# Kernel tuning notes

Measured on AMD Instinct MI355X. Metric: run time of the kernel, lower is better.

The kernel has to match this reference:

```python
import jax, jax.numpy as jnp
import numpy as np

N_CELLS = 1024
HID = 256
IN_DIM = 256
OUT_DIM = 256
NOISE_DIM = 32
N_LOOP = 32  # min(32, n_cells)


def _lin(x, W, b):
    # torch nn.Linear: y = x @ W.T + b, W shape [out, in]
    return x @ W.T + b


def faction_sync_debate(h, step, n_factions=8, sync=0.15, debate=0.15):
    n, d = h.shape
    n_f = min(n_factions, n // 2)
    if n_f < 2:
        return h
    fs = n // n_f  # assumes n_f * fs == n (true for 1024/8)
    blk = h.reshape(n_f, fs, d)
    # per-faction mean pull (disjoint slices -> order independent)
    blk = (1.0 - sync) * blk + sync * blk.mean(axis=1, keepdims=True)
    if step > 5:  # step is a Python int -> static branch
        global_opinion = blk.mean(axis=1).mean(axis=0)  # [d]
        dc = max(1, fs // 4)
        blk = blk.at[:, :dc, :].set((1.0 - debate) * blk[:, :dc, :] + debate * global_opinion)
    return blk.reshape(n, d)


def setup_inputs() -> dict:
    key = jax.random.key(0)
    ks = iter(jax.random.split(key, 32))

    def rn(shape, scale=0.02):
        return (jax.random.normal(next(ks), shape, dtype=jnp.float32) * scale)

    flat = N_CELLS * HID  # 262144
    inp = {
        "x": rn((1, IN_DIM), 1.0),
        "noise": rn((1, NOISE_DIM), 1.0),
        "cell_hiddens": rn((N_CELLS, HID), 0.1),
        # generator: Linear(in+32,256) -> ReLU -> Linear(256,512) -> ReLU -> Linear(512, flat)
        "gen_W1": rn((256, IN_DIM + NOISE_DIM)), "gen_b1": rn((256,)),
        "gen_W2": rn((512, 256)), "gen_b2": rn((512,)),
        "gen_W3": rn((flat, 512)), "gen_b3": rn((flat,)),
        # discriminator: Linear(flat,512) -> LReLU(0.2) -> Linear(512,256) -> LReLU -> Linear(256,1) -> Sigmoid
        "disc_W1": rn((512, flat)), "disc_b1": rn((512,)),
        "disc_W2": rn((256, 512)), "disc_b2": rn((256,)),
        "disc_W3": rn((1, 256)), "disc_b3": rn((1,)),
        # mind engines: Linear(in+hid,128) -> ReLU -> Linear(128,out)
        "ea_W1": rn((128, IN_DIM + HID)), "ea_b1": rn((128,)),
        "ea_W2": rn((OUT_DIM, 128)), "ea_b2": rn((OUT_DIM,)),
        "eg_W1": rn((128, IN_DIM + HID)), "eg_b1": rn((128,)),
        "eg_W2": rn((OUT_DIM, 128)), "eg_b2": rn((OUT_DIM,)),
        # GRUCell(out+1, hid): gate order r, z, n
        "gru_Wih": rn((3 * HID, OUT_DIM + 1)), "gru_bih": rn((3 * HID,)),
        "gru_Whh": rn((3 * HID, HID)), "gru_bhh": rn((3 * HID,)),
        "step": 10,
    }
    return inp


def reference(x, noise, cell_hiddens,
              gen_W1, gen_b1, gen_W2, gen_b2, gen_W3, gen_b3,
              disc_W1, disc_b1, disc_W2, disc_b2, disc_W3, disc_b3,
              ea_W1, ea_b1, ea_W2, ea_b2, eg_W1, eg_b1, eg_W2, eg_b2,
              gru_Wih, gru_bih, gru_Whh, gru_bhh, step):
    sg = jax.lax.stop_gradient
    # --- generate_states ---
    gi = jnp.concatenate([x, noise], axis=-1)           # [1, in+32]
    h1 = jax.nn.relu(_lin(gi, gen_W1, gen_b1))
    h2 = jax.nn.relu(_lin(h1, gen_W2, gen_b2))
    gen_states = _lin(h2, gen_W3, gen_b3).reshape(N_CELLS, HID)
    # torch: gen_states.detach() then faction sync+debate
    synced = faction_sync_debate(sg(gen_states), step)
    # --- batched BenchMind over first 32 cells (replaces Python loop) ---
    H = synced[:N_LOOP]                                  # [32, HID]
    X = jnp.broadcast_to(x, (N_LOOP, x.shape[-1]))       # [32, IN]
    comb = jnp.concatenate([X, H], axis=-1)              # [32, IN+HID]
    a = _lin(jax.nn.relu(_lin(comb, ea_W1, ea_b1)), ea_W2, ea_b2)
    g = _lin(jax.nn.relu(_lin(comb, eg_W1, eg_b1)), eg_W2, eg_b2)
    outputs = a - g                                      # [32, OUT]
    tensions = (outputs ** 2).mean(axis=-1)              # [32]
    # GRUCell update (mem inputs detached as in torch)
    mem_in = jnp.concatenate([sg(outputs), sg(tensions)[:, None]], axis=-1)  # [32, OUT+1]
    gih = _lin(mem_in, gru_Wih, gru_bih)
    ghh = _lin(H, gru_Whh, gru_bhh)
    ir, iz, i_n = jnp.split(gih, 3, axis=-1)
    hr, hz, h_n = jnp.split(ghh, 3, axis=-1)
    r = jax.nn.sigmoid(ir + hr)
    z = jax.nn.sigmoid(iz + hz)
    n_cand = jnp.tanh(i_n + r * h_n)
    new_hiddens = (1.0 - z) * n_cand + z * H             # [32, HID]
    # --- buffer update (no_grad) + discriminate ---
    new_cell_hiddens = sg(0.7 * synced + 0.3 * cell_hiddens)

    def disc(s):
        f = s.reshape(1, -1)
        d1 = jax.nn.leaky_relu(_lin(f, disc_W1, disc_b1), 0.2)
        d2 = jax.nn.leaky_relu(_lin(d1, disc_W2, disc_b2), 0.2)
        return jax.nn.sigmoid(_lin(d2, disc_W3, disc_b3))

    d_real = disc(new_cell_hiddens)
    d_fake = disc(gen_states)
    # tensions were .item()'d in torch -> constants
    mean_tension = sg(tensions).mean()
    w = jax.nn.softmax(sg(tensions))                     # [32]
    combined = (w[:, None] * outputs).sum(axis=0, keepdims=True)  # [1, OUT]
    return combined, mean_tension, d_real, d_fake, new_hiddens
```

## Files before the change

kernel.cpp:

```cpp
#include <hip/hip_runtime.h>
#include <math.h>

#define N_CELLS 1024
#define HID     256
#define IN_DIM  256
#define NOISE_DIM 32
#define OUT_DIM 256
#define N_LOOP  32
#define FLAT    (N_CELLS*HID)

typedef float f4 __attribute__((ext_vector_type(4)));

__device__ __forceinline__ float wave_reduce64(float v) {
    #pragma unroll
    for (int m = 32; m; m >>= 1) v += __shfl_xor(v, m);
    return v;
}
__device__ __forceinline__ float dot4(float4 a, float4 b) {
    return a.x*b.x + a.y*b.y + a.z*b.z + a.w*b.w;
}
__device__ __forceinline__ float dot4v(f4 a, float4 b) {
    return a.x*b.x + a.y*b.y + a.z*b.z + a.w*b.w;
}
__device__ __forceinline__ float dot4vv(f4 a, f4 b) {
    return a.x*b.x + a.y*b.y + a.z*b.z + a.w*b.w;
}

__global__ void k_gen_h1(const float* __restrict__ x, const float* __restrict__ noise,
                         const float* __restrict__ W1, const float* __restrict__ b1,
                         float* __restrict__ h1) {
    __shared__ __align__(16) float gi[288];
    int t = threadIdx.x, l = t & 63, w = t >> 6;
    gi[t] = x[t];
    if (t < 32) gi[256 + t] = noise[t];
    __syncthreads();
    int j = blockIdx.x * 4 + w;
    const float4* wr = (const float4*)(W1 + j * 288);
    const float4* g4 = (const float4*)gi;
    float4 a = wr[l], v = g4[l];
    float acc = dot4(a, v);
    if (l < 8) {
        float4 a2 = wr[64 + l], v2 = g4[64 + l];
        acc += dot4(a2, v2);
    }
    acc = wave_reduce64(acc);
    if (l == 0) h1[j] = fmaxf(acc + b1[j], 0.f);
}

__global__ void k_gen_h2(const float* __restrict__ h1, const float* __restrict__ W2,
                         const float* __restrict__ b2, float* __restrict__ h2) {
    int t = threadIdx.x, l = t & 63, w = t >> 6;
    int j = blockIdx.x * 4 + w;
    float4 a = ((const float4*)(W2 + j * 256))[l];
    float4 v = ((const float4*)h1)[l];
    float acc = dot4(a, v);
    acc = wave_reduce64(acc);
    if (l == 0) h2[j] = fmaxf(acc + b2[j], 0.f);
}

__global__ void k_gen_big(const float* __restrict__ W3, const float* __restrict__ b3,
                          const float* __restrict__ h2, float* __restrict__ gs) {
    int t = threadIdx.x, l = t & 63, w = t >> 6;
    int r0 = blockIdx.x * 16 + w * 4;
    const float4* h24 = (const float4*)h2;
    float4 ha = h24[l], hb = h24[64 + l];
    const f4* w0 = (const f4*)(W3 + (size_t)(r0 + 0) * 512);
    const f4* w1 = (const f4*)(W3 + (size_t)(r0 + 1) * 512);
    const f4* w2 = (const f4*)(W3 + (size_t)(r0 + 2) * 512);
    const f4* w3 = (const f4*)(W3 + (size_t)(r0 + 3) * 512);
    f4 A0 = __builtin_nontemporal_load(w0 + l);
    f4 B0 = __builtin_nontemporal_load(w0 + 64 + l);
    f4 A1 = __builtin_nontemporal_load(w1 + l);
    f4 B1 = __builtin_nontemporal_load(w1 + 64 + l);
    f4 A2 = __builtin_nontemporal_load(w2 + l);
    f4 B2 = __builtin_nontemporal_load(w2 + 64 + l);
    f4 A3 = __builtin_nontemporal_load(w3 + l);
    f4 B3 = __builtin_nontemporal_load(w3 + 64 + l);
    float s0 = dot4v(A0, ha) + dot4v(B0, hb);
    float s1 = dot4v(A1, ha) + dot4v(B1, hb);
    float s2 = dot4v(A2, ha) + dot4v(B2, hb);
    float s3 = dot4v(A3, ha) + dot4v(B3, hb);
    s0 = wave_reduce64(s0);
    s1 = wave_reduce64(s1);
    s2 = wave_reduce64(s2);
    s3 = wave_reduce64(s3);
    if (l == 0) {
        float4 bv = *(const float4*)(b3 + r0);
        float4 o; o.x = s0 + bv.x; o.y = s1 + bv.y; o.z = s2 + bv.z; o.w = s3 + bv.w;
        *(float4*)(gs + r0) = o;
    }
}

__global__ void k_fmean(const float* __restrict__ gs, float* __restrict__ fmean) {
    __shared__ float part[4][64];
    int b = blockIdx.x, t = threadIdx.x;
    int f = b >> 2, q = b & 3;
    int c = q * 64 + (t & 63), rg = t >> 6;
    const float* base = gs + (size_t)(f * 128 + rg * 32) * 256 + c;
    float s0 = 0.f, s1 = 0.f, s2 = 0.f, s3 = 0.f;
    for (int i = 0; i < 32; i += 4) {
        s0 += base[(size_t)(i + 0) * 256];
        s1 += base[(size_t)(i + 1) * 256];
        s2 += base[(size_t)(i + 2) * 256];
        s3 += base[(size_t)(i + 3) * 256];
    }
    part[rg][t & 63] = (s0 + s1) + (s2 + s3);
    __syncthreads();
    if (t < 64) {
        float v = part[0][t] + part[1][t] + part[2][t] + part[3][t];
        fmean[f * 256 + q * 64 + t] = v * (1.f / 128.f);
    }
}

__global__ void k_mega(const float* __restrict__ dW1, const float* __restrict__ db1,
                       const float* __restrict__ gs, const float* __restrict__ ch,
                       const float* __restrict__ fmean, const int* __restrict__ step,
                       const float* __restrict__ x,
                       const float* __restrict__ eaW1, const float* __restrict__ eab1,
                       const float* __restrict__ eaW2, const float* __restrict__ eab2,
                       const float* __restrict__ egW1, const float* __restrict__ egb1,
                       const float* __restrict__ egW2, const float* __restrict__ egb2,
                       const float* __restrict__ Wih, const float* __restrict__ bih,
                       const float* __restrict__ Whh, const float* __restrict__ bhh,
                       float* __restrict__ d1r, float* __restrict__ d1f,
                       float* __restrict__ outputs, float* __restrict__ tensions,
                       float* __restrict__ out) {
    __shared__ float sR[16];
    __shared__ float sF[16];
    __shared__ __align__(16) float fmL[2048];
    __shared__ __align__(16) float gmL[256];
    __shared__ __align__(16) float xh[512];
    __shared__ __align__(16) float hag[256];
    __shared__ __align__(16) float outs[256];
    __shared__ float red[256];
    __shared__ float rzA[512];
    __shared__ float inb[256];
    __shared__ float hnb[256];
    __shared__ float tsh;
    int b = blockIdx.x, t = threadIdx.x, l = t & 63, w = t >> 6;
    bool deb = (*step > 5);

    if (b >= 32) {
        for (int i = t; i < 2048; i += 1024) fmL[i] = fmean[i];
        __syncthreads();
        if (t < 256) {
            float g = 0.f;
            #pragma unroll
            for (int f = 0; f < 8; ++f) g += fmL[f * 256 + t];
            gmL[t] = g * 0.125f;
        }
        __syncthreads();
        int row = b - 32;
        const f4* w4 = (const f4*)(dW1 + (size_t)row * FLAT);
        const float4* g4 = (const float4*)gs;
        const float4* c4 = (const float4*)ch;
        float aR = 0.f, aF = 0.f;
        for (int i = t; i < FLAT / 4; i += 1024) {
            int c = i >> 6, d4 = i & 63;
            f4 ww = __builtin_nontemporal_load(w4 + i);
            float4 gv = g4[i], cv = c4[i];
            float4 fmv = *(const float4*)(fmL + ((c >> 7) << 8) + d4 * 4);
            float4 v;
            v.x = 0.85f * gv.x + 0.15f * fmv.x;
            v.y = 0.85f * gv.y + 0.15f * fmv.y;
            v.z = 0.85f * gv.z + 0.15f * fmv.z;
            v.w = 0.85f * gv.w + 0.15f * fmv.w;
            if (deb && ((c & 127) < 32)) {
                float4 gm = *(const float4*)(gmL + d4 * 4);
                v.x = 0.85f * v.x + 0.15f * gm.x;
                v.y = 0.85f * v.y + 0.15f * gm.y;
                v.z = 0.85f * v.z + 0.15f * gm.z;
                v.w = 0.85f * v.w + 0.15f * gm.w;
            }
            float4 nc;
            nc.x = 0.7f * v.x + 0.3f * cv.x;
            nc.y = 0.7f * v.y + 0.3f * cv.y;
            nc.z = 0.7f * v.z + 0.3f * cv.z;
            nc.w = 0.7f * v.w + 0.3f * cv.w;
            aR += dot4v(ww, nc);
            aF += dot4v(ww, gv);
        }
        aR = wave_reduce64(aR);
        aF = wave_reduce64(aF);
        if (l == 0) { sR[w] = aR; sF[w] = aF; }
        __syncthreads();
        if (t < 16) {
            float r = sR[t], f = sF[t];
            #pragma unroll
            for (int m = 8; m; m >>= 1) { r += __shfl_xor(r, m); f += __shfl_xor(f, m); }
            if (t == 0) { d1r[row] = r + db1[row]; d1f[row] = f + db1[row]; }
        }
        return;
    }

    int i = b;
    if (t < 256) {
        xh[t] = x[t];
        float g = gs[i * 256 + t];
        float gmv = 0.f;
        #pragma unroll
        for (int f = 0; f < 8; ++f) gmv += fmean[f * 256 + t];
        gmv *= 0.125f;
        float v = 0.85f * g + 0.15f * fmean[t];
        if (deb) v = 0.85f * v + 0.15f * gmv;
        xh[256 + t] = v;
    }
    __syncthreads();

    for (int k = 0; k < 16; ++k) {
        int j = w * 16 + k;
        const float* W = (j < 128) ? (eaW1 + (size_t)j * 512) : (egW1 + (size_t)(j - 128) * 512);
        const float4* w4 = (const float4*)W;
        const float4* v4 = (const float4*)xh;
        float acc = dot4(w4[l], v4[l]) + dot4(w4[64 + l], v4[64 + l]);
        acc = wave_reduce64(acc);
        if (l == 0) {
            float bias = (j < 128) ? eab1[j] : egb1[j - 128];
            hag[j] = fmaxf(acc + bias, 0.f);
        }
    }
    __syncthreads();

    for (int k = 0; k < 16; ++k) {
        int tr = w * 16 + k;
        int sl = l & 31;
        bool lo = (l < 32);
        const float4* wv4 = lo ? (const float4*)(eaW2 + (size_t)tr * 128)
                               : (const float4*)(egW2 + (size_t)tr * 128);
        const float4* h4 = (const float4*)(hag + (lo ? 0 : 128));
        float d_ = dot4(wv4[sl], h4[sl]);
        float acc = lo ? d_ : -d_;
        acc = wave_reduce64(acc);
        if (l == 0) {
            float o = acc + eab2[tr] - egb2[tr];
            outs[tr] = o;
            outputs[i * 256 + tr] = o;
        }
    }
    __syncthreads();

    if (t < 256) red[t] = outs[t] * outs[t];
    __syncthreads();
    for (int m = 128; m; m >>= 1) { if (t < m && t + m < 256) red[t] += red[t + m]; __syncthreads(); }
    if (t == 0) { float tn = red[0] * (1.f / 256.f); tensions[i] = tn; tsh = tn; }
    __syncthreads();
    float tn = tsh;

    {
        float4 ov = ((const float4*)outs)[l];
        float4 Hv = ((const float4*)(xh + 256))[l];
        for (int k = 0; k < 48; ++k) {
            int u = w * 48 + k;
            const float* wr = Wih + (size_t)u * 257;
            float g0 = wr[4*l]*ov.x + wr[4*l+1]*ov.y + wr[4*l+2]*ov.z + wr[4*l+3]*ov.w;
            if (l == 0) g0 += wr[256] * tn;
            float4 wh = ((const float4*)(Whh + (size_t)u * 256))[l];
            float h0 = dot4(wh, Hv);
            if (u < 512) {
                float s = wave_reduce64(g0 + h0);
                if (l == 0) rzA[u] = s + bih[u] + bhh[u];
            } else {
                float sg = wave_reduce64(g0);
                float sh = wave_reduce64(h0);
                if (l == 0) { inb[u - 512] = sg + bih[u]; hnb[u - 512] = sh + bhh[u]; }
            }
        }
    }
    __syncthreads();

    if (t < 256) {
        float r = 1.f / (1.f + expf(-rzA[t]));
        float z = 1.f / (1.f + expf(-rzA[256 + t]));
        float nc = tanhf(inb[t] + r * hnb[t]);
        float Hd = xh[256 + t];
        out[259 + i * 256 + t] = (1.f - z) * nc + z * Hd;
    }
}

__global__ void k_epi1(const float* __restrict__ W2, const float* __restrict__ b2,
                       const float* __restrict__ d1r, const float* __restrict__ d1f,
                       float* __restrict__ l2buf) {
    __shared__ __align__(16) float lv[512];
    int b = blockIdx.x, t = threadIdx.x, l = t & 63, w = t >> 6;
    int br = b >> 2, q = b & 3;
    const float* d1 = br ? d1f : d1r;
    for (int j = t; j < 512; j += 256) { float v = d1[j]; lv[j] = v > 0.f ? v : 0.2f * v; }
    __syncthreads();
    const float4* l4 = (const float4*)lv;
    float4 va = l4[l], vb = l4[64 + l];
    for (int k = 0; k < 16; ++k) {
        int tr = q * 64 + w * 16 + k;
        const float4* wr = (const float4*)(W2 + (size_t)tr * 512);
        float acc = dot4(wr[l], va) + dot4(wr[64 + l], vb);
        acc = wave_reduce64(acc);
        if (l == 0) {
            float z = acc + b2[tr];
            l2buf[br * 256 + tr] = z > 0.f ? z : 0.2f * z;
        }
    }
}

__global__ void k_epi2(const float* __restrict__ W3, const float* __restrict__ b3,
                       const float* __restrict__ l2buf,
                       const float* __restrict__ outputs, const float* __restrict__ tensions,
                       float* __restrict__ out) {
    __shared__ float red[256];
    __shared__ float w[32];
    __shared__ float ts[32];
    int t = threadIdx.x;
    for (int p = 0; p < 2; ++p) {
        red[t] = l2buf[p * 256 + t] * W3[t];
        __syncthreads();
        for (int m = 128; m; m >>= 1) { if (t < m) red[t] += red[t + m]; __syncthreads(); }
        if (t == 0) out[257 + p] = 1.f / (1.f + expf(-(red[0] + b3[0])));
        __syncthreads();
    }
    if (t < 32) ts[t] = tensions[t];
    __syncthreads();
    if (t == 0) {
        float mx = ts[0];
        for (int i = 1; i < 32; ++i) mx = fmaxf(mx, ts[i]);
        float s = 0.f, mean = 0.f;
        for (int i = 0; i < 32; ++i) { float e = expf(ts[i] - mx); w[i] = e; s += e; mean += ts[i]; }
        float inv = 1.f / s;
        for (int i = 0; i < 32; ++i) w[i] *= inv;
        out[256] = mean * (1.f / 32.f);
    }
    __syncthreads();
    float c = 0.f;
    for (int i = 0; i < 32; ++i) c += w[i] * outputs[i * 256 + t];
    out[t] = c;
}

extern "C" void kernel_launch(void* const* d_in, const int* in_sizes, int n_in,
                              void* d_out, int out_size, void* d_ws, size_t ws_size,
                              hipStream_t stream) {
    const float* x     = (const float*)d_in[0];
    const float* noise = (const float*)d_in[1];
    const float* ch    = (const float*)d_in[2];
    const float* gW1   = (const float*)d_in[3];
    const float* gb1   = (const float*)d_in[4];
    const float* gW2   = (const float*)d_in[5];
    const float* gb2   = (const float*)d_in[6];
    const float* gW3   = (const float*)d_in[7];
    const float* gb3   = (const float*)d_in[8];
    const float* dW1   = (const float*)d_in[9];
    const float* db1   = (const float*)d_in[10];
    const float* dW2   = (const float*)d_in[11];
    const float* db2   = (const float*)d_in[12];
    const float* dW3   = (const float*)d_in[13];
    const float* db3   = (const float*)d_in[14];
    const float* eaW1  = (const float*)d_in[15];
    const float* eab1  = (const float*)d_in[16];
    const float* eaW2  = (const float*)d_in[17];
    const float* eab2  = (const float*)d_in[18];
    const float* egW1  = (const float*)d_in[19];
    const float* egb1  = (const float*)d_in[20];
    const float* egW2  = (const float*)d_in[21];
    const float* egb2  = (const float*)d_in[22];
    const float* Wih   = (const float*)d_in[23];
    const float* bih   = (const float*)d_in[24];
    const float* Whh   = (const float*)d_in[25];
    const float* bhh   = (const float*)d_in[26];
    const int*   step  = (const int*)d_in[27];

    float* out = (float*)d_out;
    float* ws  = (float*)d_ws;
    float* h1buf    = ws;
    float* h2       = h1buf + 256;
    float* gs       = h2 + 512;
    float* fmean    = gs + 262144;
    float* outputs  = fmean + 2048;
    float* tensions = outputs + 8192;
    float* d1r      = tensions + 32;
    float* d1f      = d1r + 512;
    float* l2buf    = d1f + 512;

    k_gen_h1<<<64, 256, 0, stream>>>(x, noise, gW1, gb1, h1buf);
    k_gen_h2<<<128, 256, 0, stream>>>(h1buf, gW2, gb2, h2);
    k_gen_big<<<FLAT / 16, 256, 0, stream>>>(gW3, gb3, h2, gs);
    k_fmean<<<32, 256, 0, stream>>>(gs, fmean);
    k_mega<<<544, 1024, 0, stream>>>(dW1, db1, gs, ch, fmean, step, x,
                                     eaW1, eab1, eaW2, eab2,
                                     egW1, egb1, egW2, egb2,
                                     Wih, bih, Whh, bhh,
                                     d1r, d1f, outputs, tensions, out);
    k_epi1<<<8, 256, 0, stream>>>(dW2, db2, d1r, d1f, l2buf);
    k_epi2<<<1, 256, 0, stream>>>(dW3, db3, l2buf, outputs, tensions, out);
}
```

Baseline: 274.2 us.

## Fuse generator GEMV, faction means and discriminator into one flag-synchronized kernel

Merges the big generator GEMV, the per-faction mean and the discriminator/GRU work into one persistent-style launch. Interleaved consumer blocks wait on per-faction atomic flags, so streaming the 512MB discriminator weights overlaps with streaming the generator weights. Each discriminator block now handles two rows and shares the gs/ch loads between them. The synced state is folded algebraically into the dot-product coefficients, with a separate debate-sum correction. The cost is spin-wait dependencies on block scheduling order, which can deadlock or stall if consumer blocks occupy all slots before their producers run, plus relaxed atomic loads of gs.

```diff
diff --git a/kernel.cpp b/kernel.cpp
--- a/kernel.cpp
+++ b/kernel.cpp
@@ -3,11 +3,11 @@
 
 #define N_CELLS 1024
 #define HID     256
-#define IN_DIM  256
-#define NOISE_DIM 32
-#define OUT_DIM 256
 #define N_LOOP  32
 #define FLAT    (N_CELLS*HID)
+
+#define GRIDF   4384
+#define NSPEC   288
 
 typedef float f4 __attribute__((ext_vector_type(4)));
 
@@ -22,27 +22,24 @@
 __device__ __forceinline__ float dot4v(f4 a, float4 b) {
     return a.x*b.x + a.y*b.y + a.z*b.z + a.w*b.w;
 }
-__device__ __forceinline__ float dot4vv(f4 a, f4 b) {
-    return a.x*b.x + a.y*b.y + a.z*b.z + a.w*b.w;
-}
+
+#define ALD(p)   __hip_atomic_load((p), __ATOMIC_RELAXED, __HIP_MEMORY_SCOPE_AGENT)
+#define AST(p,v) __hip_atomic_store((p), (v), __ATOMIC_RELAXED, __HIP_MEMORY_SCOPE_AGENT)
 
 __global__ void k_gen_h1(const float* __restrict__ x, const float* __restrict__ noise,
                          const float* __restrict__ W1, const float* __restrict__ b1,
-                         float* __restrict__ h1) {
+                         float* __restrict__ h1, unsigned int* __restrict__ ctrl) {
     __shared__ __align__(16) float gi[288];
     int t = threadIdx.x, l = t & 63, w = t >> 6;
+    if (blockIdx.x == 0 && t < 64) ctrl[t] = 0u;
     gi[t] = x[t];
     if (t < 32) gi[256 + t] = noise[t];
     __syncthreads();
     int j = blockIdx.x * 4 + w;
     const float4* wr = (const float4*)(W1 + j * 288);
     const float4* g4 = (const float4*)gi;
-    float4 a = wr[l], v = g4[l];
-    float acc = dot4(a, v);
-    if (l < 8) {
-        float4 a2 = wr[64 + l], v2 = g4[64 + l];
-        acc += dot4(a2, v2);
-    }
+    float acc = dot4(wr[l], g4[l]);
+    if (l < 8) acc += dot4(wr[64 + l], g4[64 + l]);
     acc = wave_reduce64(acc);
     if (l == 0) h1[j] = fmaxf(acc + b1[j], 0.f);
 }
@@ -51,229 +48,296 @@
                          const float* __restrict__ b2, float* __restrict__ h2) {
     int t = threadIdx.x, l = t & 63, w = t >> 6;
     int j = blockIdx.x * 4 + w;
-    float4 a = ((const float4*)(W2 + j * 256))[l];
-    float4 v = ((const float4*)h1)[l];
-    float acc = dot4(a, v);
+    float acc = dot4(((const float4*)(W2 + j * 256))[l], ((const float4*)h1)[l]);
     acc = wave_reduce64(acc);
     if (l == 0) h2[j] = fmaxf(acc + b2[j], 0.f);
 }
 
-__global__ void k_gen_big(const float* __restrict__ W3, const float* __restrict__ b3,
-                          const float* __restrict__ h2, float* __restrict__ gs) {
-    int t = threadIdx.x, l = t & 63, w = t >> 6;
-    int r0 = blockIdx.x * 16 + w * 4;
-    const float4* h24 = (const float4*)h2;
-    float4 ha = h24[l], hb = h24[64 + l];
-    const f4* w0 = (const f4*)(W3 + (size_t)(r0 + 0) * 512);
-    const f4* w1 = (const f4*)(W3 + (size_t)(r0 + 1) * 512);
-    const f4* w2 = (const f4*)(W3 + (size_t)(r0 + 2) * 512);
-    const f4* w3 = (const f4*)(W3 + (size_t)(r0 + 3) * 512);
-    f4 A0 = __builtin_nontemporal_load(w0 + l);
-    f4 B0 = __builtin_nontemporal_load(w0 + 64 + l);
-    f4 A1 = __builtin_nontemporal_load(w1 + l);
-    f4 B1 = __builtin_nontemporal_load(w1 + 64 + l);
-    f4 A2 = __builtin_nontemporal_load(w2 + l);
-    f4 B2 = __builtin_nontemporal_load(w2 + 64 + l);
-    f4 A3 = __builtin_nontemporal_load(w3 + l);
-    f4 B3 = __builtin_nontemporal_load(w3 + 64 + l);
-    float s0 = dot4v(A0, ha) + dot4v(B0, hb);
-    float s1 = dot4v(A1, ha) + dot4v(B1, hb);
-    float s2 = dot4v(A2, ha) + dot4v(B2, hb);
-    float s3 = dot4v(A3, ha) + dot4v(B3, hb);
-    s0 = wave_reduce64(s0);
-    s1 = wave_reduce64(s1);
-    s2 = wave_reduce64(s2);
-    s3 = wave_reduce64(s3);
-    if (l == 0) {
-        float4 bv = *(const float4*)(b3 + r0);
-        float4 o; o.x = s0 + bv.x; o.y = s1 + bv.y; o.z = s2 + bv.z; o.w = s3 + bv.w;
-        *(float4*)(gs + r0) = o;
-    }
-}
-
-__global__ void k_fmean(const float* __restrict__ gs, float* __restrict__ fmean) {
-    __shared__ float part[4][64];
-    int b = blockIdx.x, t = threadIdx.x;
-    int f = b >> 2, q = b & 3;
-    int c = q * 64 + (t & 63), rg = t >> 6;
-    const float* base = gs + (size_t)(f * 128 + rg * 32) * 256 + c;
-    float s0 = 0.f, s1 = 0.f, s2 = 0.f, s3 = 0.f;
-    for (int i = 0; i < 32; i += 4) {
-        s0 += base[(size_t)(i + 0) * 256];
-        s1 += base[(size_t)(i + 1) * 256];
-        s2 += base[(size_t)(i + 2) * 256];
-        s3 += base[(size_t)(i + 3) * 256];
-    }
-    part[rg][t & 63] = (s0 + s1) + (s2 + s3);
-    __syncthreads();
-    if (t < 64) {
-        float v = part[0][t] + part[1][t] + part[2][t] + part[3][t];
-        fmean[f * 256 + q * 64 + t] = v * (1.f / 128.f);
-    }
-}
-
-__global__ void k_mega(const float* __restrict__ dW1, const float* __restrict__ db1,
-                       const float* __restrict__ gs, const float* __restrict__ ch,
-                       const float* __restrict__ fmean, const int* __restrict__ step,
-                       const float* __restrict__ x,
-                       const float* __restrict__ eaW1, const float* __restrict__ eab1,
-                       const float* __restrict__ eaW2, const float* __restrict__ eab2,
-                       const float* __restrict__ egW1, const float* __restrict__ egb1,
-                       const float* __restrict__ egW2, const float* __restrict__ egb2,
-                       const float* __restrict__ Wih, const float* __restrict__ bih,
-                       const float* __restrict__ Whh, const float* __restrict__ bhh,
-                       float* __restrict__ d1r, float* __restrict__ d1f,
-                       float* __restrict__ outputs, float* __restrict__ tensions,
-                       float* __restrict__ out) {
-    __shared__ float sR[16];
-    __shared__ float sF[16];
+__global__ void __launch_bounds__(1024, 8)
+k_fused(const float* __restrict__ W3, const float* __restrict__ b3,
+        const float* __restrict__ h2,
+        const float* __restrict__ dW1, const float* __restrict__ db1,
+        const float* __restrict__ ch, const int* __restrict__ step,
+        const float* __restrict__ x,
+        const float* __restrict__ eaW1, const float* __restrict__ eab1,
+        const float* __restrict__ eaW2, const float* __restrict__ eab2,
+        const float* __restrict__ egW1, const float* __restrict__ egb1,
+        const float* __restrict__ egW2, const float* __restrict__ egb2,
+        const float* __restrict__ Wih, const float* __restrict__ bih,
+        const float* __restrict__ Whh, const float* __restrict__ bhh,
+        float* __restrict__ gs, float* __restrict__ fmean,
+        unsigned int* __restrict__ ctrl,
+        float* __restrict__ d1r, float* __restrict__ d1f,
+        float* __restrict__ outputs, float* __restrict__ tensions,
+        float* __restrict__ out) {
     __shared__ __align__(16) float fmL[2048];
     __shared__ __align__(16) float gmL[256];
-    __shared__ __align__(16) float xh[512];
+    __shared__ __align__(16) float swl[4096];
+    __shared__ float swS[256];
+    __shared__ float sA[16], sB[16], sC[16], sD[16];
+    __shared__ float sS[2];
+    __shared__ __align__(16) float fm_part[1024];
+    __shared__ int lastS;
+    __shared__ __align__(16) float xL[256];
+    __shared__ __align__(16) float vf[256];
+    __shared__ float Hacc[256];
+    __shared__ float E[256];
+    __shared__ float Ghh[768];
     __shared__ __align__(16) float hag[256];
     __shared__ __align__(16) float outs[256];
     __shared__ float red[256];
-    __shared__ float rzA[512];
-    __shared__ float inb[256];
-    __shared__ float hnb[256];
+    __shared__ float gihL[768];
     __shared__ float tsh;
+
+    unsigned int* fcnt  = ctrl;
+    unsigned int* fflag = ctrl + 32;
     int b = blockIdx.x, t = threadIdx.x, l = t & 63, w = t >> 6;
     bool deb = (*step > 5);
 
-    if (b >= 32) {
-        for (int i = t; i < 2048; i += 1024) fmL[i] = fmean[i];
+    int s = -1;
+    if ((b % 15) == 0 && (b / 15) < NSPEC) s = b / 15;
+
+    if (s < 0) {
+        int nb = (b == 0) ? 0 : ((b - 1) / 15 + 1);
+        if (nb > NSPEC) nb = NSPEC;
+        int g = b - nb;
+        int fct = g >> 9;
+        int r0 = g * 64 + w * 4;
+        const float4* h24 = (const float4*)h2;
+        float4 ha = h24[l], hb = h24[64 + l];
+        const f4* w0p = (const f4*)(W3 + (size_t)(r0 + 0) * 512);
+        const f4* w1p = (const f4*)(W3 + (size_t)(r0 + 1) * 512);
+        const f4* w2p = (const f4*)(W3 + (size_t)(r0 + 2) * 512);
+        const f4* w3p = (const f4*)(W3 + (size_t)(r0 + 3) * 512);
+        f4 A0 = __builtin_nontemporal_load(w0p + l), B0 = __builtin_nontemporal_load(w0p + 64 + l);
+        f4 A1 = __builtin_nontemporal_load(w1p + l), B1 = __builtin_nontemporal_load(w1p + 64 + l);
+        f4 A2 = __builtin_nontemporal_load(w2p + l), B2 = __builtin_nontemporal_load(w2p + 64 + l);
+        f4 A3 = __builtin_nontemporal_load(w3p + l), B3 = __builtin_nontemporal_load(w3p + 64 + l);
+        float s0 = dot4v(A0, ha) + dot4v(B0, hb);
+        float s1 = dot4v(A1, ha) + dot4v(B1, hb);
+        float s2 = dot4v(A2, ha) + dot4v(B2, hb);
+        float s3 = dot4v(A3, ha) + dot4v(B3, hb);
+        s0 = wave_reduce64(s0); s1 = wave_reduce64(s1);
+        s2 = wave_reduce64(s2); s3 = wave_reduce64(s3);
+        if (l < 4) {
+            float sv = (l == 0) ? s0 : (l == 1) ? s1 : (l == 2) ? s2 : s3;
+            AST(gs + r0 + l, sv + b3[r0 + l]);
+        }
+        __syncthreads();
+        if (t == 0)
+            lastS = (__hip_atomic_fetch_add(&fcnt[fct], 1u, __ATOMIC_ACQ_REL,
+                                            __HIP_MEMORY_SCOPE_AGENT) == 511u);
+        __syncthreads();
+        if (lastS) {
+            int d = t & 255, q = t >> 8;
+            const float* basep = gs + fct * 32768 + q * 8192 + d;
+            float sum = 0.f;
+            for (int r = 0; r < 32; ++r) sum += ALD(basep + r * 256);
+            fm_part[t] = sum;
+            __syncthreads();
+            if (t < 256) {
+                float v = (fm_part[t] + fm_part[256 + t] + fm_part[512 + t] + fm_part[768 + t])
+                          * (1.f / 128.f);
+                AST(fmean + fct * 256 + t, v);
+            }
+            __syncthreads();
+            if (t == 0)
+                __hip_atomic_store(&fflag[fct], 1u, __ATOMIC_RELEASE, __HIP_MEMORY_SCOPE_AGENT);
+        }
+        return;
+    }
+
+    if (s < 256) {
+        int row0 = 2 * s, row1 = 2 * s + 1;
+        const f4* wr0 = (const f4*)dW1 + (size_t)row0 * 65536;
+        const f4* wr1 = (const f4*)dW1 + (size_t)row1 * 65536;
+        const float4* c4 = (const float4*)ch;
+        float aR0 = 0.f, aF0 = 0.f, aR1 = 0.f, aF1 = 0.f;
+        f4 SW0 = {0.f, 0.f, 0.f, 0.f}, SW1 = {0.f, 0.f, 0.f, 0.f};
+        for (int f = 0; f < 8; ++f) {
+            if (t == 0) {
+                while (__hip_atomic_load(&fflag[f], __ATOMIC_ACQUIRE,
+                                         __HIP_MEMORY_SCOPE_AGENT) == 0u)
+                    __builtin_amdgcn_s_sleep(16);
+            }
+            __syncthreads();
+            if (t < 256) fmL[f * 256 + t] = ALD(fmean + f * 256 + t);
+            __syncthreads();
+            int base = f * 8192;
+            #pragma unroll 2
+            for (int k2 = 0; k2 < 8; ++k2) {
+                int i = base + k2 * 1024 + t;
+                f4 ww0 = __builtin_nontemporal_load(wr0 + i);
+                f4 ww1 = __builtin_nontemporal_load(wr1 + i);
+                const float* gp = gs + 4 * (size_t)i;
+                float g0 = ALD(gp + 0), g1 = ALD(gp + 1), g2 = ALD(gp + 2), g3 = ALD(gp + 3);
+                float4 cv = c4[i];
+                f4 fmv = ((const f4*)fmL)[(f << 6) + (i & 63)];
+                bool debate = deb && (((i >> 6) & 127) < 32);
+                float cg = debate ? 0.50575f : 0.595f;
+                float cf = debate ? 0.08925f : 0.105f;
+                float dg0 = ww0.x*g0 + ww0.y*g1 + ww0.z*g2 + ww0.w*g3;
+                float df0 = ww0.x*fmv.x + ww0.y*fmv.y + ww0.z*fmv.z + ww0.w*fmv.w;
+                float dc0 = ww0.x*cv.x + ww0.y*cv.y + ww0.z*cv.z + ww0.w*cv.w;
+                aR0 += cg*dg0 + cf*df0 + 0.3f*dc0;  aF0 += dg0;
+                float dg1 = ww1.x*g0 + ww1.y*g1 + ww1.z*g2 + ww1.w*g3;
+                float df1 = ww1.x*fmv.x + ww1.y*fmv.y + ww1.z*fmv.z + ww1.w*fmv.w;
+                float dc1 = ww1.x*cv.x + ww1.y*cv.y + ww1.z*cv.z + ww1.w*cv.w;
+                aR1 += cg*dg1 + cf*df1 + 0.3f*dc1;  aF1 += dg1;
+                if (debate) { SW0 += ww0; SW1 += ww1; }
+            }
+        }
         __syncthreads();
         if (t < 256) {
-            float g = 0.f;
+            float gsum = 0.f;
             #pragma unroll
-            for (int f = 0; f < 8; ++f) g += fmL[f * 256 + t];
-            gmL[t] = g * 0.125f;
-        }
-        __syncthreads();
-        int row = b - 32;
-        const f4* w4 = (const f4*)(dW1 + (size_t)row * FLAT);
-        const float4* g4 = (const float4*)gs;
-        const float4* c4 = (const float4*)ch;
-        float aR = 0.f, aF = 0.f;
-        for (int i = t; i < FLAT / 4; i += 1024) {
-            int c = i >> 6, d4 = i & 63;
-            f4 ww = __builtin_nontemporal_load(w4 + i);
-            float4 gv = g4[i], cv = c4[i];
-            float4 fmv = *(const float4*)(fmL + ((c >> 7) << 8) + d4 * 4);
-            float4 v;
-            v.x = 0.85f * gv.x + 0.15f * fmv.x;
-            v.y = 0.85f * gv.y + 0.15f * fmv.y;
-            v.z = 0.85f * gv.z + 0.15f * fmv.z;
-            v.w = 0.85f * gv.w + 0.15f * fmv.w;
-            if (deb && ((c & 127) < 32)) {
-                float4 gm = *(const float4*)(gmL + d4 * 4);
-                v.x = 0.85f * v.x + 0.15f * gm.x;
-                v.y = 0.85f * v.y + 0.15f * gm.y;
-                v.z = 0.85f * v.z + 0.15f * gm.z;
-                v.w = 0.85f * v.w + 0.15f * gm.w;
-            }
-            float4 nc;
-            nc.x = 0.7f * v.x + 0.3f * cv.x;
-            nc.y = 0.7f * v.y + 0.3f * cv.y;
-            nc.z = 0.7f * v.z + 0.3f * cv.z;
-            nc.w = 0.7f * v.w + 0.3f * cv.w;
-            aR += dot4v(ww, nc);
-            aF += dot4v(ww, gv);
-        }
-        aR = wave_reduce64(aR);
-        aF = wave_reduce64(aF);
-        if (l == 0) { sR[w] = aR; sF[w] = aF; }
+            for (int f = 0; f < 8; ++f) gsum += fmL[f * 256 + t];
+            gmL[t] = gsum * 0.125f;
+        }
+        __syncthreads();
+        ((f4*)swl)[w * 64 + l] = SW0;
+        __syncthreads();
+        if (t < 256) {
+            float sv = 0.f;
+            #pragma unroll
+            for (int q = 0; q < 16; ++q) sv += swl[q * 256 + t];
+            swS[t] = sv * gmL[t];
+        }
+        __syncthreads();
+        for (int m = 128; m; m >>= 1) { if (t < m) swS[t] += swS[t + m]; __syncthreads(); }
+        if (t == 0) sS[0] = swS[0];
+        __syncthreads();
+        ((f4*)swl)[w * 64 + l] = SW1;
+        __syncthreads();
+        if (t < 256) {
+            float sv = 0.f;
+            #pragma unroll
+            for (int q = 0; q < 16; ++q) sv += swl[q * 256 + t];
+            swS[t] = sv * gmL[t];
+        }
+        __syncthreads();
+        for (int m = 128; m; m >>= 1) { if (t < m) swS[t] += swS[t + m]; __syncthreads(); }
+        if (t == 0) sS[1] = swS[0];
+        __syncthreads();
+        aR0 = wave_reduce64(aR0); aF0 = wave_reduce64(aF0);
+        aR1 = wave_reduce64(aR1); aF1 = wave_reduce64(aF1);
+        if (l == 0) { sA[w] = aR0; sB[w] = aF0; sC[w] = aR1; sD[w] = aF1; }
         __syncthreads();
         if (t < 16) {
-            float r = sR[t], f = sF[t];
+            float a = sA[t], bb = sB[t], c = sC[t], dd = sD[t];
             #pragma unroll
-            for (int m = 8; m; m >>= 1) { r += __shfl_xor(r, m); f += __shfl_xor(f, m); }
-            if (t == 0) { d1r[row] = r + db1[row]; d1f[row] = f + db1[row]; }
+            for (int m = 8; m; m >>= 1) {
+                a += __shfl_xor(a, m); bb += __shfl_xor(bb, m);
+                c += __shfl_xor(c, m); dd += __shfl_xor(dd, m);
+            }
+            if (t == 0) {
+                d1r[row0] = a + 0.105f * sS[0] + db1[row0];
+                d1f[row0] = bb + db1[row0];
+                d1r[row1] = c + 0.105f * sS[1] + db1[row1];
+                d1f[row1] = dd + db1[row1];
+            }
         }
         return;
     }
 
-    int i = b;
-    if (t < 256) {
-        xh[t] = x[t];
-        float g = gs[i * 256 + t];
-        float gmv = 0.f;
-        #pragma unroll
-        for (int f = 0; f < 8; ++f) gmv += fmean[f * 256 + t];
-        gmv *= 0.125f;
-        float v = 0.85f * g + 0.15f * fmean[t];
-        if (deb) v = 0.85f * v + 0.15f * gmv;
-        xh[256 + t] = v;
-    }
-    __syncthreads();
-
-    for (int k = 0; k < 16; ++k) {
-        int j = w * 16 + k;
-        const float* W = (j < 128) ? (eaW1 + (size_t)j * 512) : (egW1 + (size_t)(j - 128) * 512);
-        const float4* w4 = (const float4*)W;
-        const float4* v4 = (const float4*)xh;
-        float acc = dot4(w4[l], v4[l]) + dot4(w4[64 + l], v4[64 + l]);
-        acc = wave_reduce64(acc);
-        if (l == 0) {
-            float bias = (j < 128) ? eab1[j] : egb1[j - 128];
-            hag[j] = fmaxf(acc + bias, 0.f);
-        }
-    }
-    __syncthreads();
-
-    for (int k = 0; k < 16; ++k) {
-        int tr = w * 16 + k;
-        int sl = l & 31;
-        bool lo = (l < 32);
-        const float4* wv4 = lo ? (const float4*)(eaW2 + (size_t)tr * 128)
-                               : (const float4*)(egW2 + (size_t)tr * 128);
-        const float4* h4 = (const float4*)(hag + (lo ? 0 : 128));
-        float d_ = dot4(wv4[sl], h4[sl]);
-        float acc = lo ? d_ : -d_;
-        acc = wave_reduce64(acc);
-        if (l == 0) {
-            float o = acc + eab2[tr] - egb2[tr];
-            outs[tr] = o;
-            outputs[i * 256 + tr] = o;
-        }
-    }
-    __syncthreads();
-
-    if (t < 256) red[t] = outs[t] * outs[t];
-    __syncthreads();
-    for (int m = 128; m; m >>= 1) { if (t < m && t + m < 256) red[t] += red[t + m]; __syncthreads(); }
-    if (t == 0) { float tn = red[0] * (1.f / 256.f); tensions[i] = tn; tsh = tn; }
-    __syncthreads();
-    float tn = tsh;
-
     {
-        float4 ov = ((const float4*)outs)[l];
-        float4 Hv = ((const float4*)(xh + 256))[l];
-        for (int k = 0; k < 48; ++k) {
-            int u = w * 48 + k;
-            const float* wr = Wih + (size_t)u * 257;
-            float g0 = wr[4*l]*ov.x + wr[4*l+1]*ov.y + wr[4*l+2]*ov.z + wr[4*l+3]*ov.w;
-            if (l == 0) g0 += wr[256] * tn;
-            float4 wh = ((const float4*)(Whh + (size_t)u * 256))[l];
-            float h0 = dot4(wh, Hv);
-            if (u < 512) {
-                float s = wave_reduce64(g0 + h0);
-                if (l == 0) rzA[u] = s + bih[u] + bhh[u];
-            } else {
-                float sg = wave_reduce64(g0);
-                float sh = wave_reduce64(h0);
-                if (l == 0) { inb[u - 512] = sg + bih[u]; hnb[u - 512] = sh + bhh[u]; }
-            }
-        }
-    }
-    __syncthreads();
-
-    if (t < 256) {
-        float r = 1.f / (1.f + expf(-rzA[t]));
-        float z = 1.f / (1.f + expf(-rzA[256 + t]));
-        float nc = tanhf(inb[t] + r * hnb[t]);
-        float Hd = xh[256 + t];
-        out[259 + i * 256 + t] = (1.f - z) * nc + z * Hd;
+        int i = s - 256;
+        if (t < 256) { xL[t] = x[t]; Hacc[t] = 0.f; }
+        for (int j2 = t; j2 < 768; j2 += 1024) Ghh[j2] = 0.f;
+        __syncthreads();
+        for (int k = 0; k < 16; ++k) {
+            int j = w * 16 + k;
+            const float* Wp = (j < 128) ? (eaW1 + (size_t)j * 512)
+                                        : (egW1 + (size_t)(j - 128) * 512);
+            float acc = dot4(((const float4*)Wp)[l], ((const float4*)xL)[l]);
+            acc = wave_reduce64(acc);
+            if (l == 0) E[j] = acc;
+        }
+        int nf = deb ? 8 : 1;
+        for (int f = 0; f < nf; ++f) {
+            if (t == 0) {
+                while (__hip_atomic_load(&fflag[f], __ATOMIC_ACQUIRE,
+                                         __HIP_MEMORY_SCOPE_AGENT) == 0u)
+                    __builtin_amdgcn_s_sleep(16);
+            }
+            __syncthreads();
+            if (t < 256) {
+                float fmv = ALD(fmean + f * 256 + t);
+                float v;
+                if (f == 0) {
+                    float gsv = ALD(gs + i * 256 + t);
+                    v = deb ? (0.7225f * gsv + 0.14625f * fmv)
+                            : (0.85f * gsv + 0.15f * fmv);
+                } else {
+                    v = 0.01875f * fmv;
+                }
+                vf[t] = v;
+                Hacc[t] += v;
+            }
+            __syncthreads();
+            for (int k = 0; k < 16; ++k) {
+                int j = w * 16 + k;
+                const float* Wp = (j < 128) ? (eaW1 + (size_t)j * 512 + 256)
+                                            : (egW1 + (size_t)(j - 128) * 512 + 256);
+                float acc = dot4(((const float4*)Wp)[l], ((const float4*)vf)[l]);
+                acc = wave_reduce64(acc);
+                if (l == 0) E[j] += acc;
+            }
+            for (int k = 0; k < 48; ++k) {
+                int u = w * 48 + k;
+                float acc = dot4(((const float4*)(Whh + (size_t)u * 256))[l],
+                                 ((const float4*)vf)[l]);
+                acc = wave_reduce64(acc);
+                if (l == 0) Ghh[u] += acc;
+            }
+            __syncthreads();
+        }
+        if (t < 256) {
+            float e = E[t] + ((t < 128) ? eab1[t] : egb1[t - 128]);
+            hag[t] = fmaxf(e, 0.f);
+        }
+        __syncthreads();
+        for (int k = 0; k < 16; ++k) {
+            int tr = w * 16 + k;
+            int sl = l & 31;
+            bool lo = (l < 32);
+            const float4* wv4 = lo ? (const float4*)(eaW2 + (size_t)tr * 128)
+                                   : (const float4*)(egW2 + (size_t)tr * 128);
+            const float4* h4 = (const float4*)(hag + (lo ? 0 : 128));
+            float d_ = dot4(wv4[sl], h4[sl]);
+            float acc = lo ? d_ : -d_;
+            acc = wave_reduce64(acc);
+            if (l == 0) {
+                float o = acc + eab2[tr] - egb2[tr];
+                outs[tr] = o;
+                outputs[i * 256 + tr] = o;
+            }
+        }
+        __syncthreads();
+        if (t < 256) red[t] = outs[t] * outs[t];
+        __syncthreads();
+        for (int m = 128; m; m >>= 1) { if (t < m) red[t] += red[t + m]; __syncthreads(); }
+        if (t == 0) { float tn = red[0] * (1.f / 256.f); tensions[i] = tn; tsh = tn; }
+        __syncthreads();
+        float tn = tsh;
+        {
+            float4 ov = ((const float4*)outs)[l];
+            for (int k = 0; k < 48; ++k) {
+                int u = w * 48 + k;
+                const float* wr = Wih + (size_t)u * 257;
+                float g0 = wr[4*l]*ov.x + wr[4*l+1]*ov.y + wr[4*l+2]*ov.z + wr[4*l+3]*ov.w;
+                if (l == 0) g0 += wr[256] * tn;
+                g0 = wave_reduce64(g0);
+                if (l == 0) gihL[u] = g0 + bih[u];
+            }
+        }
+        __syncthreads();
+        if (t < 256) {
+            float rr = 1.f / (1.f + expf(-(gihL[t] + Ghh[t] + bhh[t])));
+            float zz = 1.f / (1.f + expf(-(gihL[256 + t] + Ghh[256 + t] + bhh[256 + t])));
+            float ncand = tanhf(gihL[512 + t] + rr * (Ghh[512 + t] + bhh[512 + t]));
+            out[259 + i * 256 + t] = (1.f - zz) * ncand + zz * Hacc[t];
+        }
     }
 }
 
@@ -375,16 +439,17 @@
     float* d1r      = tensions + 32;
     float* d1f      = d1r + 512;
     float* l2buf    = d1f + 512;
-
-    k_gen_h1<<<64, 256, 0, stream>>>(x, noise, gW1, gb1, h1buf);
+    unsigned int* ctrl = (unsigned int*)(l2buf + 512);
+
+    k_gen_h1<<<64, 256, 0, stream>>>(x, noise, gW1, gb1, h1buf, ctrl);
     k_gen_h2<<<128, 256, 0, stream>>>(h1buf, gW2, gb2, h2);
-    k_gen_big<<<FLAT / 16, 256, 0, stream>>>(gW3, gb3, h2, gs);
-    k_fmean<<<32, 256, 0, stream>>>(gs, fmean);
-    k_mega<<<544, 1024, 0, stream>>>(dW1, db1, gs, ch, fmean, step, x,
-                                     eaW1, eab1, eaW2, eab2,
-                                     egW1, egb1, egW2, egb2,
-                                     Wih, bih, Whh, bhh,
-                                     d1r, d1f, outputs, tensions, out);
+    k_fused<<<GRIDF, 1024, 0, stream>>>(gW3, gb3, h2,
+                                        dW1, db1, ch, step, x,
+                                        eaW1, eab1, eaW2, eab2,
+                                        egW1, egb1, egW2, egb2,
+                                        Wih, bih, Whh, bhh,
+                                        gs, fmean, ctrl,
+                                        d1r, d1f, outputs, tensions, out);
     k_epi1<<<8, 256, 0, stream>>>(dW2, db2, d1r, d1f, l2buf);
     k_epi2<<<1, 256, 0, stream>>>(dW3, db3, l2buf, outputs, tensions, out);
 }
```

Measured after the change: 709.2 us. 2.59x slower.

## Process two discriminator rows per block over half the columns to reuse state loads

Applied to the files above, without the earlier changes.

Each discriminator block now handles two weight rows over half of the flattened input instead of one full row, so the recomputed synced/new-hidden values and gs/ch loads are shared across two rows. Partial sums for each half are written to scratch, and the bias add plus the combining of the halves move into k_epi1. k_fmean is also rewritten to use 8 blocks with float4 column reads. The intent is to cut redundant reads of gs/ch and their elementwise recomputation, which dominate next to the 512MB dW1 stream. The cost is more registers per thread and less parallelism in k_fmean.

```diff
diff --git a/kernel.cpp b/kernel.cpp
--- a/kernel.cpp
+++ b/kernel.cpp
@@ -3,9 +3,6 @@
 
 #define N_CELLS 1024
 #define HID     256
-#define IN_DIM  256
-#define NOISE_DIM 32
-#define OUT_DIM 256
 #define N_LOOP  32
 #define FLAT    (N_CELLS*HID)
 
@@ -37,12 +34,8 @@
     int j = blockIdx.x * 4 + w;
     const float4* wr = (const float4*)(W1 + j * 288);
     const float4* g4 = (const float4*)gi;
-    float4 a = wr[l], v = g4[l];
-    float acc = dot4(a, v);
-    if (l < 8) {
-        float4 a2 = wr[64 + l], v2 = g4[64 + l];
-        acc += dot4(a2, v2);
-    }
+    float acc = dot4(wr[l], g4[l]);
+    if (l < 8) acc += dot4(wr[64 + l], g4[64 + l]);
     acc = wave_reduce64(acc);
     if (l == 0) h1[j] = fmaxf(acc + b1[j], 0.f);
 }
@@ -51,9 +44,7 @@
                          const float* __restrict__ b2, float* __restrict__ h2) {
     int t = threadIdx.x, l = t & 63, w = t >> 6;
     int j = blockIdx.x * 4 + w;
-    float4 a = ((const float4*)(W2 + j * 256))[l];
-    float4 v = ((const float4*)h1)[l];
-    float acc = dot4(a, v);
+    float acc = dot4(((const float4*)(W2 + j * 256))[l], ((const float4*)h1)[l]);
     acc = wave_reduce64(acc);
     if (l == 0) h2[j] = fmaxf(acc + b2[j], 0.f);
 }
@@ -92,23 +83,18 @@
 }
 
 __global__ void k_fmean(const float* __restrict__ gs, float* __restrict__ fmean) {
-    __shared__ float part[4][64];
-    int b = blockIdx.x, t = threadIdx.x;
-    int f = b >> 2, q = b & 3;
-    int c = q * 64 + (t & 63), rg = t >> 6;
-    const float* base = gs + (size_t)(f * 128 + rg * 32) * 256 + c;
-    float s0 = 0.f, s1 = 0.f, s2 = 0.f, s3 = 0.f;
-    for (int i = 0; i < 32; i += 4) {
-        s0 += base[(size_t)(i + 0) * 256];
-        s1 += base[(size_t)(i + 1) * 256];
-        s2 += base[(size_t)(i + 2) * 256];
-        s3 += base[(size_t)(i + 3) * 256];
-    }
-    part[rg][t & 63] = (s0 + s1) + (s2 + s3);
+    __shared__ __align__(16) f4 part[4][64];
+    int f = blockIdx.x, t = threadIdx.x;
+    int rg = t >> 6, c4 = t & 63;
+    const f4* base = (const f4*)(gs + (size_t)(f * 128 + rg * 32) * 256) + c4;
+    f4 acc = {0.f, 0.f, 0.f, 0.f};
+    for (int r = 0; r < 32; ++r) acc += base[r * 64];
+    part[rg][c4] = acc;
     __syncthreads();
     if (t < 64) {
-        float v = part[0][t] + part[1][t] + part[2][t] + part[3][t];
-        fmean[f * 256 + q * 64 + t] = v * (1.f / 128.f);
+        f4 v = (part[0][t] + part[1][t]) + (part[2][t] + part[3][t]);
+        v *= (1.f / 128.f);
+        *(f4*)(fmean + f * 256 + t * 4) = v;
     }
 }
 
@@ -122,11 +108,10 @@
                        const float* __restrict__ egW2, const float* __restrict__ egb2,
                        const float* __restrict__ Wih, const float* __restrict__ bih,
                        const float* __restrict__ Whh, const float* __restrict__ bhh,
-                       float* __restrict__ d1r, float* __restrict__ d1f,
+                       float* __restrict__ d1rp, float* __restrict__ d1fp,
                        float* __restrict__ outputs, float* __restrict__ tensions,
                        float* __restrict__ out) {
-    __shared__ float sR[16];
-    __shared__ float sF[16];
+    __shared__ float sA[16], sB[16], sC[16], sD[16];
     __shared__ __align__(16) float fmL[2048];
     __shared__ __align__(16) float gmL[256];
     __shared__ __align__(16) float xh[512];
@@ -150,14 +135,20 @@
             gmL[t] = g * 0.125f;
         }
         __syncthreads();
-        int row = b - 32;
-        const f4* w4 = (const f4*)(dW1 + (size_t)row * FLAT);
+        int idx = b - 32;
+        int p = idx >> 1, half = idx & 1;
+        int row0 = 2 * p, row1 = 2 * p + 1;
+        const f4* wr0 = (const f4*)dW1 + (size_t)row0 * 65536;
+        const f4* wr1 = (const f4*)dW1 + (size_t)row1 * 65536;
         const float4* g4 = (const float4*)gs;
         const float4* c4 = (const float4*)ch;
-        float aR = 0.f, aF = 0.f;
-        for (int i = t; i < FLAT / 4; i += 1024) {
+        int kbase = half * 32768;
+        float aR0 = 0.f, aF0 = 0.f, aR1 = 0.f, aF1 = 0.f;
+        for (int k = 0; k < 32; ++k) {
+            int i = kbase + k * 1024 + t;
+            f4 ww0 = __builtin_nontemporal_load(wr0 + i);
+            f4 ww1 = __builtin_nontemporal_load(wr1 + i);
             int c = i >> 6, d4 = i & 63;
-            f4 ww = __builtin_nontemporal_load(w4 + i);
             float4 gv = g4[i], cv = c4[i];
             float4 fmv = *(const float4*)(fmL + ((c >> 7) << 8) + d4 * 4);
             float4 v;
@@ -177,18 +168,28 @@
             nc.y = 0.7f * v.y + 0.3f * cv.y;
             nc.z = 0.7f * v.z + 0.3f * cv.z;
             nc.w = 0.7f * v.w + 0.3f * cv.w;
-            aR += dot4v(ww, nc);
-            aF += dot4v(ww, gv);
-        }
-        aR = wave_reduce64(aR);
-        aF = wave_reduce64(aF);
-        if (l == 0) { sR[w] = aR; sF[w] = aF; }
+            aR0 += dot4v(ww0, nc);
+            aF0 += dot4v(ww0, gv);
+            aR1 += dot4v(ww1, nc);
+            aF1 += dot4v(ww1, gv);
+        }
+        aR0 = wave_reduce64(aR0); aF0 = wave_reduce64(aF0);
+        aR1 = wave_reduce64(aR1); aF1 = wave_reduce64(aF1);
+        if (l == 0) { sA[w] = aR0; sB[w] = aF0; sC[w] = aR1; sD[w] = aF1; }
         __syncthreads();
         if (t < 16) {
-            float r = sR[t], f = sF[t];
+            float a = sA[t], bb = sB[t], c = sC[t], dd = sD[t];
             #pragma unroll
-            for (int m = 8; m; m >>= 1) { r += __shfl_xor(r, m); f += __shfl_xor(f, m); }
-            if (t == 0) { d1r[row] = r + db1[row]; d1f[row] = f + db1[row]; }
+            for (int m = 8; m; m >>= 1) {
+                a += __shfl_xor(a, m); bb += __shfl_xor(bb, m);
+                c += __shfl_xor(c, m); dd += __shfl_xor(dd, m);
+            }
+            if (t == 0) {
+                d1rp[half * 512 + row0] = a;
+                d1fp[half * 512 + row0] = bb;
+                d1rp[half * 512 + row1] = c;
+                d1fp[half * 512 + row1] = dd;
+            }
         }
         return;
     }
@@ -278,13 +279,17 @@
 }
 
 __global__ void k_epi1(const float* __restrict__ W2, const float* __restrict__ b2,
-                       const float* __restrict__ d1r, const float* __restrict__ d1f,
+                       const float* __restrict__ db1,
+                       const float* __restrict__ d1rp, const float* __restrict__ d1fp,
                        float* __restrict__ l2buf) {
     __shared__ __align__(16) float lv[512];
     int b = blockIdx.x, t = threadIdx.x, l = t & 63, w = t >> 6;
     int br = b >> 2, q = b & 3;
-    const float* d1 = br ? d1f : d1r;
-    for (int j = t; j < 512; j += 256) { float v = d1[j]; lv[j] = v > 0.f ? v : 0.2f * v; }
+    const float* dp = br ? d1fp : d1rp;
+    for (int j = t; j < 512; j += 256) {
+        float v = dp[j] + dp[512 + j] + db1[j];
+        lv[j] = v > 0.f ? v : 0.2f * v;
+    }
     __syncthreads();
     const float4* l4 = (const float4*)lv;
     float4 va = l4[l], vb = l4[64 + l];
@@ -372,19 +377,19 @@
     float* fmean    = gs + 262144;
     float* outputs  = fmean + 2048;
     float* tensions = outputs + 8192;
-    float* d1r      = tensions + 32;
-    float* d1f      = d1r + 512;
-    float* l2buf    = d1f + 512;
+    float* d1rp     = tensions + 32;
+    float* d1fp     = d1rp + 1024;
+    float* l2buf    = d1fp + 1024;
 
     k_gen_h1<<<64, 256, 0, stream>>>(x, noise, gW1, gb1, h1buf);
     k_gen_h2<<<128, 256, 0, stream>>>(h1buf, gW2, gb2, h2);
     k_gen_big<<<FLAT / 16, 256, 0, stream>>>(gW3, gb3, h2, gs);
-    k_fmean<<<32, 256, 0, stream>>>(gs, fmean);
+    k_fmean<<<8, 256, 0, stream>>>(gs, fmean);
     k_mega<<<544, 1024, 0, stream>>>(dW1, db1, gs, ch, fmean, step, x,
                                      eaW1, eab1, eaW2, eab2,
                                      egW1, egb1, egW2, egb2,
                                      Wih, bih, Whh, bhh,
-                                     d1r, d1f, outputs, tensions, out);
-    k_epi1<<<8, 256, 0, stream>>>(dW2, db2, d1r, d1f, l2buf);
+                                     d1rp, d1fp, outputs, tensions, out);
+    k_epi1<<<8, 256, 0, stream>>>(dW2, db2, db1, d1rp, d1fp, l2buf);
     k_epi2<<<1, 256, 0, stream>>>(dW3, db3, l2buf, outputs, tensions, out);
 }
```

Result: slower. 643.5 us (+134.7%).
